# Kernel optimization log

Measured on AMD Instinct MI355X. Metric: run time of the kernel, lower is better.

The kernel has to match this reference:

```python
import jax, jax.numpy as jnp
import numpy as np

C = 1.0          # Poincare ball curvature
EPS = 1e-7
MAX_TANH_ARG = 1.0 - 1e-5
K = 5            # topk neighbors (hardcoded in the module)


def _norm(x):
    return jnp.clip(jnp.linalg.norm(x, axis=-1, keepdims=True), EPS)


def expmap0(u):
    # exp map at origin: tanh(sqrt(c)||u||) * u / (sqrt(c)||u||)
    sc = jnp.sqrt(C)
    n = _norm(u)
    return jnp.tanh(sc * n) * u / (sc * n)


def logmap0(x):
    # log map at origin: artanh(sqrt(c)||x||) * x / (sqrt(c)||x||)
    sc = jnp.sqrt(C)
    n = _norm(x)
    arg = jnp.clip(sc * n, EPS, MAX_TANH_ARG)
    return jnp.arctanh(arg) * x / (sc * n)


def mobius_add(x, y):
    x2 = jnp.sum(x * x, axis=-1, keepdims=True)
    y2 = jnp.sum(y * y, axis=-1, keepdims=True)
    xy = jnp.sum(x * y, axis=-1, keepdims=True)
    num = (1.0 + 2.0 * C * xy + C * y2) * x + (1.0 - C * x2) * y
    den = 1.0 + 2.0 * C * xy + (C * C) * x2 * y2
    return num / (den + EPS)


def setup_inputs() -> dict:
    key = jax.random.key(0)
    k1, k2, k3, k4 = jax.random.split(key, 4)
    B, SEQ_DIM, HYP_DIM, N = 2048, 768, 128, 100000
    z_seq = jax.random.normal(k1, (B, SEQ_DIM), dtype=jnp.float32)
    # node embeddings must lie inside the unit ball; scale keeps norms ~0.57
    node_emb = 0.05 * jax.random.normal(k2, (N, HYP_DIM), dtype=jnp.float32)
    W = 0.02 * jax.random.normal(k3, (HYP_DIM, SEQ_DIM), dtype=jnp.float32)
    b = jnp.zeros((HYP_DIM,), dtype=jnp.float32)
    return {"z_seq": z_seq, "node_emb": node_emb, "W": W, "b": b}


def reference(z_seq, node_emb, W, b):
    # linear projection (dropout is identity in eval mode)
    z_proj = z_seq @ W.T + b                     # (B, D)
    z_hyp = expmap0(z_proj)                      # (B, D) in Poincare ball
    # no-grad nearest-node lookup in tangent space
    z_tan = logmap0(z_hyp)                       # (B, D)
    n_tan = logmap0(node_emb)                    # (N, D)
    # squared euclidean distances (monotone in cdist -> same topk indices)
    d2 = (jnp.sum(z_tan * z_tan, axis=-1, keepdims=True)
          - 2.0 * (z_tan @ n_tan.T)
          + jnp.sum(n_tan * n_tan, axis=-1)[None, :])  # (B, N)
    _, idx = jax.lax.top_k(-d2, K)               # (B, K) smallest distances
    near = jnp.mean(node_emb[idx], axis=1)       # (B, D) gather-mean
    z_fused = mobius_add(z_hyp, near)
    return (z_fused, z_hyp)
```

## Files before the change

### kernel.cpp

```cpp
#include <hip/hip_runtime.h>
#include <hip/hip_bf16.h>
#include <math.h>

#define EPSF 1e-7f
#define MAXT 0.99999f

typedef __attribute__((ext_vector_type(8))) short short8v;
typedef __attribute__((ext_vector_type(4))) float f32x4;

constexpr int Bb = 2048;
constexpr int Ss = 768;
constexpr int Dd = 128;
constexpr int Nn = 100000;
constexpr int Kk = 5;
constexpr int HALF = Bb * Dd;
constexpr int NT = 128;
constexpr int TILE_BYTES = NT * Dd * 2;
constexpr int SUP_BYTES = 2 * TILE_BYTES;
constexpr float SBIAS = 16.0f;

constexpr int NCH8 = 8;
constexpr int CH8 = Nn / NCH8;
constexpr int TIL8 = 98;
constexpr int NSUP = TIL8 / 2;
constexpr int PAD8 = TIL8 * NT;
constexpr int RQ = 64;

constexpr int NCH16 = 16;
constexpr int CH16 = Nn / NCH16;
constexpr int TIL16 = (CH16 + NT - 1) / NT;
constexpr int RT = 128;

static __device__ __forceinline__ ushort f2bf(float x) {
  __hip_bfloat16 h = __float2bfloat16(x);
  return *reinterpret_cast<ushort*>(&h);
}

static __device__ __forceinline__ float med3f(float a, float b, float c) {
  float r;
  asm("v_med3_f32 %0, %1, %2, %3" : "=v"(r) : "v"(a), "v"(b), "v"(c));
  return r;
}

static __device__ __forceinline__ void ins5f(float* k, float v) {
  const float n0 = fminf(k[0], v);
  const float n1 = med3f(k[0], k[1], v);
  const float n2 = med3f(k[1], k[2], v);
  const float n3 = med3f(k[2], k[3], v);
  const float n4 = med3f(k[3], k[4], v);
  k[0] = n0; k[1] = n1; k[2] = n2; k[3] = n3; k[4] = n4;
}

#define INS5(TV, TI, V, ID) do { \
  const float _v = (V); const int _id = (ID); \
  if (_v < TV[4]) { \
    TV[4] = _v; TI[4] = _id; \
    if (TV[4] < TV[3]) { float _t=TV[3];TV[3]=TV[4];TV[4]=_t;int _u=TI[3];TI[3]=TI[4];TI[4]=_u; } \
    if (TV[3] < TV[2]) { float _t=TV[2];TV[2]=TV[3];TV[3]=_t;int _u=TI[2];TI[2]=TI[3];TI[3]=_u; } \
    if (TV[2] < TV[1]) { float _t=TV[1];TV[1]=TV[2];TV[2]=_t;int _u=TI[1];TI[1]=TI[2];TI[2]=_u; } \
    if (TV[1] < TV[0]) { float _t=TV[0];TV[0]=TV[1];TV[1]=_t;int _u=TI[0];TI[0]=TI[1];TI[1]=_u; } \
  } } while(0)

#define LXLT(V,I,V2,I2) ((V) < (V2) || ((V) == (V2) && (I) < (I2)))
#define INS5L(TV, TI, V, ID) do { \
  const float _v = (V); const int _id = (ID); \
  if (LXLT(_v,_id,TV[4],TI[4])) { \
    TV[4]=_v; TI[4]=_id; \
    if (LXLT(TV[4],TI[4],TV[3],TI[3])) { float _t=TV[3];TV[3]=TV[4];TV[4]=_t;int _u=TI[3];TI[3]=TI[4];TI[4]=_u; } \
    if (LXLT(TV[3],TI[3],TV[2],TI[2])) { float _t=TV[2];TV[2]=TV[3];TV[3]=_t;int _u=TI[2];TI[2]=TI[3];TI[3]=_u; } \
    if (LXLT(TV[2],TI[2],TV[1],TI[1])) { float _t=TV[1];TV[1]=TV[2];TV[2]=_t;int _u=TI[1];TI[1]=TI[2];TI[2]=_u; } \
    if (LXLT(TV[1],TI[1],TV[0],TI[0])) { float _t=TV[0];TV[0]=TV[1];TV[1]=_t;int _u=TI[0];TI[0]=TI[1];TI[1]=_u; } \
  } } while(0)

static __device__ __forceinline__ void proj_body(
    const float* __restrict__ zseq, const float* __restrict__ W,
    const float* __restrict__ bias, float* __restrict__ outH,
    ushort* __restrict__ ztb, int blk,
    float (*zrow)[768], float (*zp)[128], float (*php)[128], float* rno)
{
  const int tid = threadIdx.x;
  const int d = tid & 127, h = tid >> 7;
  const int r0 = blk * 8;

  {
    const float4* src = reinterpret_cast<const float4*>(zseq + (size_t)r0 * Ss);
    float4* dst = reinterpret_cast<float4*>(&zrow[0][0]);
    #pragma unroll
    for (int i = 0; i < 6; ++i) dst[i * 256 + tid] = src[i * 256 + tid];
  }
  __syncthreads();

  float acc[8];
  #pragma unroll
  for (int r = 0; r < 8; ++r) acc[r] = 0.f;
  const float4* w4 = reinterpret_cast<const float4*>(W + (size_t)d * Ss) + h * 96;
  for (int j = 0; j < 96; ++j) {
    const float4 w = w4[j];
    const int kb = h * 384 + j * 4;
    #pragma unroll
    for (int r = 0; r < 8; ++r) {
      const float4 z = *reinterpret_cast<const float4*>(&zrow[r][kb]);
      acc[r] = fmaf(z.x, w.x, acc[r]);
      acc[r] = fmaf(z.y, w.y, acc[r]);
      acc[r] = fmaf(z.z, w.z, acc[r]);
      acc[r] = fmaf(z.w, w.w, acc[r]);
    }
  }
  #pragma unroll
  for (int r = 0; r < 8; ++r) {
    if (h == 0) zp[r][d] = acc[r]; else php[r][d] = acc[r];
  }
  __syncthreads();
  if (tid < 128) {
    const float bv = bias[d];
    #pragma unroll
    for (int r = 0; r < 8; ++r) zp[r][d] = zp[r][d] + php[r][d] + bv;
  }
  __syncthreads();

  const int wv = tid >> 6, ln = tid & 63;
  if (tid < 128) {
    #pragma unroll
    for (int rr = 0; rr < 4; ++rr) {
      const int r = wv * 4 + rr;
      float v = zp[r][ln] * zp[r][ln] + zp[r][ln + 64] * zp[r][ln + 64];
      #pragma unroll
      for (int off = 32; off > 0; off >>= 1) v += __shfl_xor(v, off);
      if (ln == 0) rno[r] = v;
    }
  }
  __syncthreads();
  if (tid < 128) {
    #pragma unroll
    for (int r = 0; r < 8; ++r) {
      const float n = fmaxf(sqrtf(rno[r]), EPSF);
      const float zh = tanhf(n) * zp[r][d] / n;
      outH[(size_t)(r0 + r) * Dd + d] = zh;
      zp[r][d] = zh;
    }
  }
  __syncthreads();
  if (tid < 128) {
    #pragma unroll
    for (int rr = 0; rr < 4; ++rr) {
      const int r = wv * 4 + rr;
      float v = zp[r][ln] * zp[r][ln] + zp[r][ln + 64] * zp[r][ln + 64];
      #pragma unroll
      for (int off = 32; off > 0; off >>= 1) v += __shfl_xor(v, off);
      if (ln == 0) rno[r] = v;
    }
  }
  __syncthreads();
  if (tid < 128) {
    #pragma unroll
    for (int r = 0; r < 8; ++r) {
      const float m = fmaxf(sqrtf(rno[r]), EPSF);
      const float a = atanhf(fminf(m, MAXT));
      ztb[(size_t)(r0 + r) * Dd + d] = f2bf(a * zp[r][d] / m);
    }
  }
}

__global__ __launch_bounds__(256) void k_proj(
    const float* __restrict__ zseq, const float* __restrict__ W,
    const float* __restrict__ bias, float* __restrict__ outH,
    ushort* __restrict__ ztb)
{
  __shared__ __align__(16) float zrow[8][768];
  __shared__ float zp[8][128];
  __shared__ float php[8][128];
  __shared__ float rno[8];
  proj_body(zseq, W, bias, outH, ztb, blockIdx.x, zrow, zp, php, rno);
}

__global__ __launch_bounds__(256) void k_prep(
    const float* __restrict__ zseq, const float* __restrict__ W,
    const float* __restrict__ bias, float* __restrict__ outH,
    ushort* __restrict__ ztb, const float* __restrict__ emb,
    ushort* __restrict__ embsw, float* __restrict__ cpad)
{
  __shared__ __align__(16) float zrow[8][768];
  __shared__ float zp[8][128];
  __shared__ float php[8][128];
  __shared__ float rno[8];

  if (blockIdx.x < Bb / 8) {
    proj_body(zseq, W, bias, outH, ztb, blockIdx.x, zrow, zp, php, rno);
    return;
  }

  const int wv = threadIdx.x >> 6, ln = threadIdx.x & 63;
  const int half = ln >> 5, l5 = ln & 31;
  const int p = (blockIdx.x - Bb / 8) * 8 + wv * 2 + half;
  const int chunk = p / PAD8;
  const int local = p - chunk * PAD8;
  const bool real = local < CH8;
  const int node = chunk * CH8 + local;
  float4 v = make_float4(0.f, 0.f, 0.f, 0.f);
  if (real) v = *reinterpret_cast<const float4*>(emb + (size_t)node * Dd + l5 * 4);
  float t = v.x * v.x + v.y * v.y + v.z * v.z + v.w * v.w;
  #pragma unroll
  for (int off = 16; off > 0; off >>= 1) t += __shfl_xor(t, off);

  const float E = fmaxf(sqrtf(t), EPSF);
  const float a = atanhf(fminf(E, MAXT));
  const float s = a / E;
  const float m2s = -2.f * s;

  const int tt = local >> 7, nd = local & 127;
  ushort4 w;
  w.x = f2bf(m2s * v.x); w.y = f2bf(m2s * v.y);
  w.z = f2bf(m2s * v.z); w.w = f2bf(m2s * v.w);
  char* dst = reinterpret_cast<char*>(embsw)
            + ((size_t)((chunk * TIL8 + tt) * NT + nd) << 8)
            + ((l5 * 8) ^ ((nd & 7) << 4));
  *reinterpret_cast<ushort4*>(dst) = w;

  if (l5 == 0) cpad[p] = real ? (s * s * t + SBIAS) : 3.0e38f;
}

__global__ __launch_bounds__(1024, 4) void k_topk8(
    const ushort* __restrict__ ztb, const ushort* __restrict__ embsw,
    const float* __restrict__ cpad, float* __restrict__ candV,
    int* __restrict__ candI)
{
  __shared__ __align__(16) ushort Bsm[2][2][NT * Dd];

  const int tid = threadIdx.x;
  const int ln = tid & 63;
  const int wv8 = (tid >> 6) & 7;
  const int qh = tid >> 9;
  const int ln15 = ln & 15;
  const int g = ln >> 4;
  const int chunk = blockIdx.x & 7;
  const int rowBase = (blockIdx.x >> 3) * RQ;
  const int qBase = rowBase + qh * 32;
  const char* embc = reinterpret_cast<const char*>(embsw)
                   + (size_t)chunk * (TIL8 * TILE_BYTES);
  const float* cch = cpad + (size_t)chunk * PAD8;

  short8v zfr[2][4];
  #pragma unroll
  for (int f = 0; f < 2; ++f)
    #pragma unroll
    for (int ks = 0; ks < 4; ++ks)
      zfr[f][ks] = *reinterpret_cast<const short8v*>(
          ztb + (size_t)(qBase + 16 * f + ln15) * Dd + 32 * ks + 8 * g);

  int rdoff[4];
  #pragma unroll
  for (int ks = 0; ks < 4; ++ks)
    rdoff[ks] = (wv8 * 16 + ln15) * 256 + ((ks * 64 + g * 16) ^ ((ln15 & 7) << 4));
  const unsigned lanebase = (unsigned)(wv8 * 16 + 4 * g);

  float tv0[5], tv1[5];
  const float KINIT = __uint_as_float(0x7F7FFFFFu);
  #pragma unroll
  for (int q = 0; q < 5; ++q) { tv0[q] = KINIT; tv1[q] = KINIT; }

  const char* srcP = embc + tid * 16;
  unsigned long long cvP =
      (unsigned long long)(cch + wv8 * 16 + 4 * g);

  f32x4 cvA0, cvA1, cvB0, cvB1;

#define STAGE(BB, CV0, CV1) do { \
    char* lb = reinterpret_cast<char*>(&Bsm[BB][0][0]) + tid * 16; \
    __builtin_amdgcn_global_load_lds( \
        (const __attribute__((address_space(1))) unsigned int*)(srcP), \
        (__attribute__((address_space(3))) unsigned int*)(lb), 16, 0, 0); \
    __builtin_amdgcn_global_load_lds( \
        (const __attribute__((address_space(1))) unsigned int*)(srcP + 16384), \
        (__attribute__((address_space(3))) unsigned int*)(lb + 16384), 16, 0, 0); \
    __builtin_amdgcn_global_load_lds( \
        (const __attribute__((address_space(1))) unsigned int*)(srcP + 32768), \
        (__attribute__((address_space(3))) unsigned int*)(lb + 32768), 16, 0, 0); \
    __builtin_amdgcn_global_load_lds( \
        (const __attribute__((address_space(1))) unsigned int*)(srcP + 49152), \
        (__attribute__((address_space(3))) unsigned int*)(lb + 49152), 16, 0, 0); \
    asm volatile("global_load_dwordx4 %0, %2, off\n\t" \
                 "global_load_dwordx4 %1, %3, off" \
        : "=&v"(CV0), "=&v"(CV1) \
        : "v"(cvP), "v"(cvP + (unsigned long long)(NT * 4))); \
    srcP += SUP_BYTES; \
    cvP += (unsigned long long)(2 * NT * 4); } while (0)

#define TILEBODY(BB, UU, CV, IBV, MM0, MM1) do { \
    const char* bbase = reinterpret_cast<const char*>(&Bsm[BB][UU][0]); \
    const short8v ae0 = *reinterpret_cast<const short8v*>(bbase + rdoff[0]); \
    const short8v ae1 = *reinterpret_cast<const short8v*>(bbase + rdoff[1]); \
    const short8v ae2 = *reinterpret_cast<const short8v*>(bbase + rdoff[2]); \
    const short8v ae3 = *reinterpret_cast<const short8v*>(bbase + rdoff[3]); \
    __builtin_amdgcn_s_setprio(1); \
    f32x4 a0 = __builtin_amdgcn_mfma_f32_16x16x32_bf16(ae0, zfr[0][0], CV, 0, 0, 0); \
    f32x4 a1 = __builtin_amdgcn_mfma_f32_16x16x32_bf16(ae0, zfr[1][0], CV, 0, 0, 0); \
    a0 = __builtin_amdgcn_mfma_f32_16x16x32_bf16(ae1, zfr[0][1], a0, 0, 0, 0); \
    a1 = __builtin_amdgcn_mfma_f32_16x16x32_bf16(ae1, zfr[1][1], a1, 0, 0, 0); \
    a0 = __builtin_amdgcn_mfma_f32_16x16x32_bf16(ae2, zfr[0][2], a0, 0, 0, 0); \
    a1 = __builtin_amdgcn_mfma_f32_16x16x32_bf16(ae2, zfr[1][2], a1, 0, 0, 0); \
    a0 = __builtin_amdgcn_mfma_f32_16x16x32_bf16(ae3, zfr[0][3], a0, 0, 0, 0); \
    a1 = __builtin_amdgcn_mfma_f32_16x16x32_bf16(ae3, zfr[1][3], a1, 0, 0, 0); \
    __builtin_amdgcn_s_setprio(0); \
    const unsigned ibv = (IBV); \
    { const float k0 = __uint_as_float((__float_as_uint(a0[0]) & 0xFFFFC000u) | ibv); \
      const float k1 = __uint_as_float((__float_as_uint(a0[1]) & 0xFFFFC000u) | (ibv + 1)); \
      const float k2 = __uint_as_float((__float_as_uint(a0[2]) & 0xFFFFC000u) | (ibv + 2)); \
      const float k3 = __uint_as_float((__float_as_uint(a0[3]) & 0xFFFFC000u) | (ibv + 3)); \
      MM0 = fminf(MM0, fminf(fminf(k0, k1), fminf(k2, k3))); } \
    { const float k0 = __uint_as_float((__float_as_uint(a1[0]) & 0xFFFFC000u) | ibv); \
      const float k1 = __uint_as_float((__float_as_uint(a1[1]) & 0xFFFFC000u) | (ibv + 1)); \
      const float k2 = __uint_as_float((__float_as_uint(a1[2]) & 0xFFFFC000u) | (ibv + 2)); \
      const float k3 = __uint_as_float((__float_as_uint(a1[3]) & 0xFFFFC000u) | (ibv + 3)); \
      MM1 = fminf(MM1, fminf(fminf(k0, k1), fminf(k2, k3))); } \
  } while (0)

#define PROCSUP(BB, CV0, CV1, ST, WN) do { \
    asm volatile("s_waitcnt vmcnt(" #WN ")" ::: "memory"); \
    __builtin_amdgcn_sched_barrier(0); \
    __builtin_amdgcn_s_barrier(); \
    float mm0 = KINIT, mm1 = KINIT; \
    TILEBODY(BB, 0, CV0, (unsigned)((2 * (ST)) * NT) + lanebase, mm0, mm1); \
    TILEBODY(BB, 1, CV1, (unsigned)((2 * (ST) + 1) * NT) + lanebase, mm0, mm1); \
    ins5f(tv0, mm0); \
    ins5f(tv1, mm1); \
    __builtin_amdgcn_s_barrier(); \
    asm volatile("" ::: "memory"); \
  } while (0)

  asm volatile("s_waitcnt vmcnt(0)" ::: "memory");
  STAGE(0, cvA0, cvA1);
  STAGE(1, cvB0, cvB1);

  for (int ss = 0; ss < 23; ++ss) {
    PROCSUP(0, cvA0, cvA1, 2 * ss, 6);
    STAGE(0, cvA0, cvA1);
    PROCSUP(1, cvB0, cvB1, 2 * ss + 1, 6);
    STAGE(1, cvB0, cvB1);
  }
  PROCSUP(0, cvA0, cvA1, 46, 6);
  STAGE(0, cvA0, cvA1);
  PROCSUP(1, cvB0, cvB1, 47, 6);
  PROCSUP(0, cvA0, cvA1, 48, 0);

#undef STAGE
#undef TILEBODY
#undef PROCSUP

  #pragma unroll
  for (int m = 16; m <= 32; m <<= 1) {
    float ov[5];
    #pragma unroll
    for (int q = 0; q < 5; ++q) ov[q] = __shfl_xor(tv0[q], m);
    #pragma unroll
    for (int q = 0; q < 5; ++q) ins5f(tv0, ov[q]);
    #pragma unroll
    for (int q = 0; q < 5; ++q) ov[q] = __shfl_xor(tv1[q], m);
    #pragma unroll
    for (int q = 0; q < 5; ++q) ins5f(tv1, ov[q]);
  }
  __syncthreads();
  float* mgk = reinterpret_cast<float*>(&Bsm[0][0][0]);
  if (ln < 16) {
    #pragma unroll
    for (int q = 0; q < 5; ++q) {
      mgk[((qh * 32 + 0 + ln) * 8 + wv8) * Kk + q] = tv0[q];
      mgk[((qh * 32 + 16 + ln) * 8 + wv8) * Kk + q] = tv1[q];
    }
  }
  __syncthreads();
  if (tid < RQ) {
    float mv[5];
    #pragma unroll
    for (int q = 0; q < 5; ++q) mv[q] = mgk[(tid * 8 + 0) * Kk + q];
    for (int w = 1; w < 8; ++w)
      #pragma unroll
      for (int q = 0; q < 5; ++q) ins5f(mv, mgk[(tid * 8 + w) * Kk + q]);
    const size_t o = ((size_t)(rowBase + tid) * NCH8 + chunk) * Kk;
    #pragma unroll
    for (int q = 0; q < 5; ++q) {
      const unsigned u = __float_as_uint(mv[q]);
      candV[o + q] = __uint_as_float(u & 0xFFFFC000u);
      candI[o + q] = chunk * CH8 + (int)(u & 0x3FFFu);
    }
  }
}

__global__ __launch_bounds__(256) void k_node(
    const float* __restrict__ emb, float* __restrict__ sArr, float* __restrict__ cArr)
{
  const int wv = threadIdx.x >> 6, ln = threadIdx.x & 63;
  const int node = blockIdx.x * 4 + wv;
  const float2 v = *reinterpret_cast<const float2*>(emb + (size_t)node * Dd + ln * 2);
  float t = v.x * v.x + v.y * v.y;
  #pragma unroll
  for (int off = 32; off > 0; off >>= 1) t += __shfl_xor(t, off);
  if (ln == 0) {
    const float E = fmaxf(sqrtf(t), EPSF);
    const float a = atanhf(fminf(E, MAXT));
    const float s = a / E;
    sArr[node] = s;
    cArr[node] = s * s * t;
  }
}

__global__ __launch_bounds__(512, 2) void k_topk16(
    const ushort* __restrict__ ztb, const float* __restrict__ emb,
    const float* __restrict__ sArr, const float* __restrict__ cArr,
    float* __restrict__ candV, int* __restrict__ candI)
{
  __shared__ __align__(16) ushort Bsm[2][NT * Dd];
  __shared__ __align__(16) float2 sclb[2][NT];
  __shared__ __align__(16) float mgv[RT][2][Kk];
  __shared__ int mgi[RT][2][Kk];

  const int tid = threadIdx.x;
  const int ln = tid & 63;
  const int wv = tid >> 6;
  const int ln15 = ln & 15;
  const int g = ln >> 4;
  const int wr = wv >> 1;
  const int wc = wv & 1;
  const int rowBase = blockIdx.x * RT;
  const int chunkStart = blockIdx.y * CH16;

  short8v afr[2][4];
  #pragma unroll
  for (int f = 0; f < 2; ++f)
    #pragma unroll
    for (int ks = 0; ks < 4; ++ks)
      afr[f][ks] = *reinterpret_cast<const short8v*>(
          ztb + (size_t)(rowBase + 32 * wr + 16 * f + ln15) * Dd + 32 * ks + 8 * g);

  int rdoff[4];
  #pragma unroll
  for (int ks = 0; ks < 4; ++ks)
    rdoff[ks] = (wc * 64 + ln15) * 256 + ((g * 16 + ks * 64) ^ ((ln15 & 7) << 4));

  f32x4 acc[2][4];
  #pragma unroll
  for (int f = 0; f < 2; ++f)
    #pragma unroll
    for (int c = 0; c < 4; ++c) acc[f][c] = (f32x4)0.f;

  float tv[8][5]; int ti[8][5];
  #pragma unroll
  for (int r = 0; r < 8; ++r)
    #pragma unroll
    for (int q = 0; q < 5; ++q) { tv[r][q] = 3.0e38f; ti[r][q] = 0x7fffffff; }

  float4 ld[8];

  auto stageLoad = [&](int t) {
    const int tStart = t * NT;
    const int left = CH16 - tStart;
    #pragma unroll
    for (int i = 0; i < 8; ++i) {
      const int flat = i * 512 + tid;
      const int nd = flat >> 5;
      float4 v = make_float4(0.f, 0.f, 0.f, 0.f);
      if (nd < left)
        v = *reinterpret_cast<const float4*>(
            emb + (size_t)(chunkStart + tStart + nd) * Dd + (flat & 31) * 4);
      ld[i] = v;
    }
  };

  auto stageWrite = [&](int t, int buf) {
    char* base = reinterpret_cast<char*>(&Bsm[buf][0]);
    #pragma unroll
    for (int i = 0; i < 8; ++i) {
      const int flat = i * 512 + tid;
      const int nd = flat >> 5;
      const int kb = (flat & 31) * 8;
      ushort4 w;
      w.x = f2bf(ld[i].x); w.y = f2bf(ld[i].y);
      w.z = f2bf(ld[i].z); w.w = f2bf(ld[i].w);
      *reinterpret_cast<ushort4*>(base + nd * 256 + (kb ^ ((nd & 7) << 4))) = w;
    }
    const int tStart = t * NT;
    const int left = CH16 - tStart;
    if (tid < NT) {
      const bool ok = tid < left;
      sclb[buf][tid] = make_float2(ok ? -2.f * sArr[chunkStart + tStart + tid] : 0.f,
                                   ok ? cArr[chunkStart + tStart + tid] : 3.0e38f);
    }
  };

  stageLoad(0);
  stageWrite(0, 0);
  __syncthreads();

  for (int t = 0; t < TIL16; ++t) {
    const int buf = t & 1;
    const bool have = (t + 1) < TIL16;
    if (have) stageLoad(t + 1);

    const char* bbase = reinterpret_cast<const char*>(&Bsm[buf][0]);
    #pragma unroll
    for (int c = 0; c < 4; ++c) {
      #pragma unroll
      for (int ks = 0; ks < 4; ++ks) {
        const short8v bfr = *reinterpret_cast<const short8v*>(bbase + c * 4096 + rdoff[ks]);
        acc[0][c] = __builtin_amdgcn_mfma_f32_16x16x32_bf16(afr[0][ks], bfr, acc[0][c], 0, 0, 0);
        acc[1][c] = __builtin_amdgcn_mfma_f32_16x16x32_bf16(afr[1][ks], bfr, acc[1][c], 0, 0, 0);
      }
    }

    if (have) stageWrite(t + 1, buf ^ 1);

    #pragma unroll
    for (int c = 0; c < 4; ++c) {
      const int nl = wc * 64 + c * 16 + ln15;
      const float2 sc2 = sclb[buf][nl];
      const int node = chunkStart + t * NT + nl;
      #pragma unroll
      for (int f = 0; f < 2; ++f) {
        #pragma unroll
        for (int i = 0; i < 4; ++i) {
          const float v = fmaf(sc2.x, acc[f][c][i], sc2.y);
          INS5(tv[f * 4 + i], ti[f * 4 + i], v, node);
        }
        acc[f][c] = (f32x4)0.f;
      }
    }
    __syncthreads();
  }

  #pragma unroll
  for (int m = 1; m <= 8; m <<= 1) {
    #pragma unroll
    for (int r = 0; r < 8; ++r) {
      float ov[5]; int oi[5];
      #pragma unroll
      for (int q = 0; q < 5; ++q) {
        ov[q] = __shfl_xor(tv[r][q], m);
        oi[q] = __shfl_xor(ti[r][q], m);
      }
      #pragma unroll
      for (int q = 0; q < 5; ++q) INS5L(tv[r], ti[r], ov[q], oi[q]);
    }
  }
  if (ln15 == 0) {
    #pragma unroll
    for (int f = 0; f < 2; ++f)
      #pragma unroll
      for (int i = 0; i < 4; ++i) {
        const int row = 32 * wr + 16 * f + 4 * g + i;
        #pragma unroll
        for (int q = 0; q < 5; ++q) {
          mgv[row][wc][q] = tv[f * 4 + i][q];
          mgi[row][wc][q] = ti[f * 4 + i][q];
        }
      }
  }
  __syncthreads();
  if (tid < RT) {
    float mv[5]; int mi[5];
    #pragma unroll
    for (int q = 0; q < 5; ++q) { mv[q] = mgv[tid][0][q]; mi[q] = mgi[tid][0][q]; }
    #pragma unroll
    for (int q = 0; q < 5; ++q) INS5L(mv, mi, mgv[tid][1][q], mgi[tid][1][q]);
    const size_t o = ((size_t)(rowBase + tid) * NCH16 + blockIdx.y) * Kk;
    #pragma unroll
    for (int q = 0; q < 5; ++q) { candV[o + q] = mv[q]; candI[o + q] = mi[q]; }
  }
}

__global__ __launch_bounds__(256) void k_fuse(
    const float* __restrict__ emb, const float* __restrict__ candV,
    const int* __restrict__ candI, const float* __restrict__ zhyp,
    float* __restrict__ out, int ncand)
{
  const int wv = threadIdx.x >> 6, ln = threadIdx.x & 63;
  const int row = blockIdx.x * 4 + wv;

  float mv[5]; int mi[5];
  #pragma unroll
  for (int q = 0; q < 5; ++q) { mv[q] = 3.0e38f; mi[q] = 0x7fffffff; }
  const size_t base = (size_t)row * ncand;
  for (int j = ln; j < ncand; j += 64) INS5L(mv, mi, candV[base + j], candI[base + j]);
  #pragma unroll
  for (int m = 1; m <= 32; m <<= 1) {
    float ov[5]; int oi[5];
    #pragma unroll
    for (int q = 0; q < 5; ++q) { ov[q] = __shfl_xor(mv[q], m); oi[q] = __shfl_xor(mi[q], m); }
    #pragma unroll
    for (int q = 0; q < 5; ++q) INS5L(mv, mi, ov[q], oi[q]);
  }
  float y0 = 0.f, y1 = 0.f;
  #pragma unroll
  for (int q = 0; q < Kk; ++q) {
    const float* e = emb + (size_t)mi[q] * Dd;
    y0 += e[ln]; y1 += e[ln + 64];
  }
  y0 *= 0.2f; y1 *= 0.2f;
  const float x0 = zhyp[(size_t)row * Dd + ln];
  const float x1 = zhyp[(size_t)row * Dd + ln + 64];
  float x2 = x0 * x0 + x1 * x1;
  float y2 = y0 * y0 + y1 * y1;
  float xy = x0 * y0 + x1 * y1;
  #pragma unroll
  for (int off = 32; off > 0; off >>= 1) {
    x2 += __shfl_xor(x2, off);
    y2 += __shfl_xor(y2, off);
    xy += __shfl_xor(xy, off);
  }
  const float ca = 1.f + 2.f * xy + y2;
  const float cb2 = 1.f - x2;
  const float den = 1.f / (1.f + 2.f * xy + x2 * y2 + EPSF);
  out[(size_t)row * Dd + ln] = (ca * x0 + cb2 * y0) * den;
  out[(size_t)row * Dd + ln + 64] = (ca * x1 + cb2 * y1) * den;
}

extern "C" void kernel_launch(void* const* d_in, const int* in_sizes, int n_in,
                              void* d_out, int out_size, void* d_ws, size_t ws_size,
                              hipStream_t stream)
{
  (void)in_sizes; (void)n_in; (void)out_size;
  const float* zseq = (const float*)d_in[0];
  const float* emb  = (const float*)d_in[1];
  const float* W    = (const float*)d_in[2];
  const float* bias = (const float*)d_in[3];
  float* out = (float*)d_out;

  const size_t ztbBytes   = (size_t)Bb * Dd * 2;
  const size_t embswBytes = (size_t)NCH8 * TIL8 * TILE_BYTES;
  const size_t cpadBytes  = (size_t)NCH8 * PAD8 * 4;
  const size_t candVBytes = (size_t)Bb * NCH8 * Kk * 4;
  const size_t needFast = ztbBytes + embswBytes + cpadBytes + 2 * candVBytes;

  if (ws_size >= needFast) {
    char* ws = (char*)d_ws;
    ushort* ztb   = (ushort*)ws;
    ushort* embsw = (ushort*)(ws + ztbBytes);
    float*  cpad  = (float*)(ws + ztbBytes + embswBytes);
    float*  candV = (float*)(ws + ztbBytes + embswBytes + cpadBytes);
    int*    candI = (int*)(ws + ztbBytes + embswBytes + cpadBytes + candVBytes);

    hipLaunchKernelGGL(k_prep, dim3(Bb / 8 + NCH8 * PAD8 / 8), dim3(256), 0,
                       stream, zseq, W, bias, out + HALF, ztb, emb, embsw, cpad);
    hipLaunchKernelGGL(k_topk8, dim3(256), dim3(1024), 0, stream,
                       ztb, embsw, cpad, candV, candI);
    hipLaunchKernelGGL(k_fuse, dim3(Bb / 4), dim3(256), 0, stream,
                       emb, candV, candI, out + HALF, out, NCH8 * Kk);
  } else {
    char* ws = (char*)d_ws;
    ushort* ztb  = (ushort*)ws;
    float* sArr  = (float*)(ws + ztbBytes);
    float* cArr  = sArr + Nn;
    float* candV = cArr + Nn;
    int*   candI = (int*)(candV + (size_t)Bb * NCH16 * Kk);

    hipLaunchKernelGGL(k_proj, dim3(Bb / 8), dim3(256), 0, stream,
                       zseq, W, bias, out + HALF, ztb);
    hipLaunchKernelGGL(k_node, dim3(Nn / 4), dim3(256), 0, stream, emb, sArr, cArr);
    hipLaunchKernelGGL(k_topk16, dim3(Bb / RT, NCH16), dim3(512), 0, stream,
                       ztb, emb, sArr, cArr, candV, candI);
    hipLaunchKernelGGL(k_fuse, dim3(Bb / 4), dim3(256), 0, stream,
                       emb, candV, candI, out + HALF, out, NCH16 * Kk);
  }
}
```

Before: 116.5 us.

## Repartition topk waves so each covers all 64 query rows on one node tile

Changes the work split in the top-k distance kernel. Before, the two half-blocks each took 32 query rows across both node tiles of a super-tile. Now each of the 16 waves takes one 16-node subtile and all 64 query rows, running four MFMA chains. This halves LDS B-fragment reads per MFMA and the per-wave bias loads, at the cost of more z-fragment registers, four running top-5 lists, a larger cross-wave merge (16 entries per row), and an ins5f per tile instead of per super-tile.

```diff
diff --git a/kernel.cpp b/kernel.cpp
--- a/kernel.cpp
+++ b/kernel.cpp
@@ -228,43 +228,42 @@
 
   const int tid = threadIdx.x;
   const int ln = tid & 63;
-  const int wv8 = (tid >> 6) & 7;
-  const int qh = tid >> 9;
+  const int w = tid >> 6;
   const int ln15 = ln & 15;
   const int g = ln >> 4;
   const int chunk = blockIdx.x & 7;
   const int rowBase = (blockIdx.x >> 3) * RQ;
-  const int qBase = rowBase + qh * 32;
   const char* embc = reinterpret_cast<const char*>(embsw)
                    + (size_t)chunk * (TIL8 * TILE_BYTES);
   const float* cch = cpad + (size_t)chunk * PAD8;
-
-  short8v zfr[2][4];
-  #pragma unroll
-  for (int f = 0; f < 2; ++f)
+  const int tu = w >> 3;
+
+  short8v zfr[4][4];
+  #pragma unroll
+  for (int f = 0; f < 4; ++f)
     #pragma unroll
     for (int ks = 0; ks < 4; ++ks)
       zfr[f][ks] = *reinterpret_cast<const short8v*>(
-          ztb + (size_t)(qBase + 16 * f + ln15) * Dd + 32 * ks + 8 * g);
+          ztb + (size_t)(rowBase + 16 * f + ln15) * Dd + 32 * ks + 8 * g);
 
   int rdoff[4];
   #pragma unroll
   for (int ks = 0; ks < 4; ++ks)
-    rdoff[ks] = (wv8 * 16 + ln15) * 256 + ((ks * 64 + g * 16) ^ ((ln15 & 7) << 4));
-  const unsigned lanebase = (unsigned)(wv8 * 16 + 4 * g);
-
-  float tv0[5], tv1[5];
+    rdoff[ks] = ((w & 7) * 16 + ln15) * 256 + ((ks * 64 + g * 16) ^ ((ln15 & 7) << 4));
+  const unsigned lanebase = (unsigned)(w * 16 + 4 * g);
+
+  float tv0[5], tv1[5], tv2[5], tv3[5];
   const float KINIT = __uint_as_float(0x7F7FFFFFu);
   #pragma unroll
-  for (int q = 0; q < 5; ++q) { tv0[q] = KINIT; tv1[q] = KINIT; }
+  for (int q = 0; q < 5; ++q) { tv0[q] = KINIT; tv1[q] = KINIT; tv2[q] = KINIT; tv3[q] = KINIT; }
 
   const char* srcP = embc + tid * 16;
   unsigned long long cvP =
-      (unsigned long long)(cch + wv8 * 16 + 4 * g);
-
-  f32x4 cvA0, cvA1, cvB0, cvB1;
-
-#define STAGE(BB, CV0, CV1) do { \
+      (unsigned long long)(cch + tu * NT + (w & 7) * 16 + 4 * g);
+
+  f32x4 cvA, cvB;
+
+#define STAGE(BB, CV) do { \
     char* lb = reinterpret_cast<char*>(&Bsm[BB][0][0]) + tid * 16; \
     __builtin_amdgcn_global_load_lds( \
         (const __attribute__((address_space(1))) unsigned int*)(srcP), \
@@ -278,15 +277,16 @@
     __builtin_amdgcn_global_load_lds( \
         (const __attribute__((address_space(1))) unsigned int*)(srcP + 49152), \
         (__attribute__((address_space(3))) unsigned int*)(lb + 49152), 16, 0, 0); \
-    asm volatile("global_load_dwordx4 %0, %2, off\n\t" \
-                 "global_load_dwordx4 %1, %3, off" \
-        : "=&v"(CV0), "=&v"(CV1) \
-        : "v"(cvP), "v"(cvP + (unsigned long long)(NT * 4))); \
+    asm volatile("global_load_dwordx4 %0, %1, off" \
+        : "=&v"(CV) : "v"(cvP)); \
     srcP += SUP_BYTES; \
     cvP += (unsigned long long)(2 * NT * 4); } while (0)
 
-#define TILEBODY(BB, UU, CV, IBV, MM0, MM1) do { \
-    const char* bbase = reinterpret_cast<const char*>(&Bsm[BB][UU][0]); \
+#define PROCSUP(BB, CV, ST, WN) do { \
+    asm volatile("s_waitcnt vmcnt(" #WN ")" ::: "memory"); \
+    __builtin_amdgcn_sched_barrier(0); \
+    __builtin_amdgcn_s_barrier(); \
+    const char* bbase = reinterpret_cast<const char*>(&Bsm[BB][tu][0]); \
     const short8v ae0 = *reinterpret_cast<const short8v*>(bbase + rdoff[0]); \
     const short8v ae1 = *reinterpret_cast<const short8v*>(bbase + rdoff[1]); \
     const short8v ae2 = *reinterpret_cast<const short8v*>(bbase + rdoff[2]); \
@@ -294,56 +294,62 @@
     __builtin_amdgcn_s_setprio(1); \
     f32x4 a0 = __builtin_amdgcn_mfma_f32_16x16x32_bf16(ae0, zfr[0][0], CV, 0, 0, 0); \
     f32x4 a1 = __builtin_amdgcn_mfma_f32_16x16x32_bf16(ae0, zfr[1][0], CV, 0, 0, 0); \
+    f32x4 a2 = __builtin_amdgcn_mfma_f32_16x16x32_bf16(ae0, zfr[2][0], CV, 0, 0, 0); \
+    f32x4 a3 = __builtin_amdgcn_mfma_f32_16x16x32_bf16(ae0, zfr[3][0], CV, 0, 0, 0); \
     a0 = __builtin_amdgcn_mfma_f32_16x16x32_bf16(ae1, zfr[0][1], a0, 0, 0, 0); \
     a1 = __builtin_amdgcn_mfma_f32_16x16x32_bf16(ae1, zfr[1][1], a1, 0, 0, 0); \
+    a2 = __builtin_amdgcn_mfma_f32_16x16x32_bf16(ae1, zfr[2][1], a2, 0, 0, 0); \
+    a3 = __builtin_amdgcn_mfma_f32_16x16x32_bf16(ae1, zfr[3][1], a3, 0, 0, 0); \
     a0 = __builtin_amdgcn_mfma_f32_16x16x32_bf16(ae2, zfr[0][2], a0, 0, 0, 0); \
     a1 = __builtin_amdgcn_mfma_f32_16x16x32_bf16(ae2, zfr[1][2], a1, 0, 0, 0); \
+    a2 = __builtin_amdgcn_mfma_f32_16x16x32_bf16(ae2, zfr[2][2], a2, 0, 0, 0); \
+    a3 = __builtin_amdgcn_mfma_f32_16x16x32_bf16(ae2, zfr[3][2], a3, 0, 0, 0); \
     a0 = __builtin_amdgcn_mfma_f32_16x16x32_bf16(ae3, zfr[0][3], a0, 0, 0, 0); \
     a1 = __builtin_amdgcn_mfma_f32_16x16x32_bf16(ae3, zfr[1][3], a1, 0, 0, 0); \
+    a2 = __builtin_amdgcn_mfma_f32_16x16x32_bf16(ae3, zfr[2][3], a2, 0, 0, 0); \
+    a3 = __builtin_amdgcn_mfma_f32_16x16x32_bf16(ae3, zfr[3][3], a3, 0, 0, 0); \
     __builtin_amdgcn_s_setprio(0); \
-    const unsigned ibv = (IBV); \
+    const unsigned ibv = (unsigned)((ST) * (2 * NT)) + lanebase; \
     { const float k0 = __uint_as_float((__float_as_uint(a0[0]) & 0xFFFFC000u) | ibv); \
       const float k1 = __uint_as_float((__float_as_uint(a0[1]) & 0xFFFFC000u) | (ibv + 1)); \
       const float k2 = __uint_as_float((__float_as_uint(a0[2]) & 0xFFFFC000u) | (ibv + 2)); \
       const float k3 = __uint_as_float((__float_as_uint(a0[3]) & 0xFFFFC000u) | (ibv + 3)); \
-      MM0 = fminf(MM0, fminf(fminf(k0, k1), fminf(k2, k3))); } \
+      ins5f(tv0, fminf(fminf(k0, k1), fminf(k2, k3))); } \
     { const float k0 = __uint_as_float((__float_as_uint(a1[0]) & 0xFFFFC000u) | ibv); \
       const float k1 = __uint_as_float((__float_as_uint(a1[1]) & 0xFFFFC000u) | (ibv + 1)); \
       const float k2 = __uint_as_float((__float_as_uint(a1[2]) & 0xFFFFC000u) | (ibv + 2)); \
       const float k3 = __uint_as_float((__float_as_uint(a1[3]) & 0xFFFFC000u) | (ibv + 3)); \
-      MM1 = fminf(MM1, fminf(fminf(k0, k1), fminf(k2, k3))); } \
-  } while (0)
-
-#define PROCSUP(BB, CV0, CV1, ST, WN) do { \
-    asm volatile("s_waitcnt vmcnt(" #WN ")" ::: "memory"); \
-    __builtin_amdgcn_sched_barrier(0); \
-    __builtin_amdgcn_s_barrier(); \
-    float mm0 = KINIT, mm1 = KINIT; \
-    TILEBODY(BB, 0, CV0, (unsigned)((2 * (ST)) * NT) + lanebase, mm0, mm1); \
-    TILEBODY(BB, 1, CV1, (unsigned)((2 * (ST) + 1) * NT) + lanebase, mm0, mm1); \
-    ins5f(tv0, mm0); \
-    ins5f(tv1, mm1); \
+      ins5f(tv1, fminf(fminf(k0, k1), fminf(k2, k3))); } \
+    { const float k0 = __uint_as_float((__float_as_uint(a2[0]) & 0xFFFFC000u) | ibv); \
+      const float k1 = __uint_as_float((__float_as_uint(a2[1]) & 0xFFFFC000u) | (ibv + 1)); \
+      const float k2 = __uint_as_float((__float_as_uint(a2[2]) & 0xFFFFC000u) | (ibv + 2)); \
+      const float k3 = __uint_as_float((__float_as_uint(a2[3]) & 0xFFFFC000u) | (ibv + 3)); \
+      ins5f(tv2, fminf(fminf(k0, k1), fminf(k2, k3))); } \
+    { const float k0 = __uint_as_float((__float_as_uint(a3[0]) & 0xFFFFC000u) | ibv); \
+      const float k1 = __uint_as_float((__float_as_uint(a3[1]) & 0xFFFFC000u) | (ibv + 1)); \
+      const float k2 = __uint_as_float((__float_as_uint(a3[2]) & 0xFFFFC000u) | (ibv + 2)); \
+      const float k3 = __uint_as_float((__float_as_uint(a3[3]) & 0xFFFFC000u) | (ibv + 3)); \
+      ins5f(tv3, fminf(fminf(k0, k1), fminf(k2, k3))); } \
     __builtin_amdgcn_s_barrier(); \
     asm volatile("" ::: "memory"); \
   } while (0)
 
   asm volatile("s_waitcnt vmcnt(0)" ::: "memory");
-  STAGE(0, cvA0, cvA1);
-  STAGE(1, cvB0, cvB1);
+  STAGE(0, cvA);
+  STAGE(1, cvB);
 
   for (int ss = 0; ss < 23; ++ss) {
-    PROCSUP(0, cvA0, cvA1, 2 * ss, 6);
-    STAGE(0, cvA0, cvA1);
-    PROCSUP(1, cvB0, cvB1, 2 * ss + 1, 6);
-    STAGE(1, cvB0, cvB1);
-  }
-  PROCSUP(0, cvA0, cvA1, 46, 6);
-  STAGE(0, cvA0, cvA1);
-  PROCSUP(1, cvB0, cvB1, 47, 6);
-  PROCSUP(0, cvA0, cvA1, 48, 0);
+    PROCSUP(0, cvA, 2 * ss, 5);
+    STAGE(0, cvA);
+    PROCSUP(1, cvB, 2 * ss + 1, 5);
+    STAGE(1, cvB);
+  }
+  PROCSUP(0, cvA, 46, 5);
+  STAGE(0, cvA);
+  PROCSUP(1, cvB, 47, 5);
+  PROCSUP(0, cvA, 48, 0);
 
 #undef STAGE
-#undef TILEBODY
 #undef PROCSUP
 
   #pragma unroll
@@ -357,24 +363,34 @@
     for (int q = 0; q < 5; ++q) ov[q] = __shfl_xor(tv1[q], m);
     #pragma unroll
     for (int q = 0; q < 5; ++q) ins5f(tv1, ov[q]);
+    #pragma unroll
+    for (int q = 0; q < 5; ++q) ov[q] = __shfl_xor(tv2[q], m);
+    #pragma unroll
+    for (int q = 0; q < 5; ++q) ins5f(tv2, ov[q]);
+    #pragma unroll
+    for (int q = 0; q < 5; ++q) ov[q] = __shfl_xor(tv3[q], m);
+    #pragma unroll
+    for (int q = 0; q < 5; ++q) ins5f(tv3, ov[q]);
   }
   __syncthreads();
   float* mgk = reinterpret_cast<float*>(&Bsm[0][0][0]);
   if (ln < 16) {
     #pragma unroll
     for (int q = 0; q < 5; ++q) {
-      mgk[((qh * 32 + 0 + ln) * 8 + wv8) * Kk + q] = tv0[q];
-      mgk[((qh * 32 + 16 + ln) * 8 + wv8) * Kk + q] = tv1[q];
+      mgk[((0 + ln) * 16 + w) * Kk + q] = tv0[q];
+      mgk[((16 + ln) * 16 + w) * Kk + q] = tv1[q];
+      mgk[((32 + ln) * 16 + w) * Kk + q] = tv2[q];
+      mgk[((48 + ln) * 16 + w) * Kk + q] = tv3[q];
     }
   }
   __syncthreads();
   if (tid < RQ) {
     float mv[5];
     #pragma unroll
-    for (int q = 0; q < 5; ++q) mv[q] = mgk[(tid * 8 + 0) * Kk + q];
-    for (int w = 1; w < 8; ++w)
-      #pragma unroll
-      for (int q = 0; q < 5; ++q) ins5f(mv, mgk[(tid * 8 + w) * Kk + q]);
+    for (int q = 0; q < 5; ++q) mv[q] = mgk[(tid * 16 + 0) * Kk + q];
+    for (int ww = 1; ww < 16; ++ww)
+      #pragma unroll
+      for (int q = 0; q < 5; ++q) ins5f(mv, mgk[(tid * 16 + ww) * Kk + q]);
     const size_t o = ((size_t)(rowBase + tid) * NCH8 + chunk) * Kk;
     #pragma unroll
     for (int q = 0; q < 5; ++q) {
```

Measured after the change: 325.2 us. +179.3%, slower.
